# Optimization experiments

Measured on AMD Instinct MI355X. Metric: run time of the kernel, lower is better.

The kernel has to match this reference:

```python
import jax, jax.numpy as jnp
import numpy as np

TOP_K = 4


def setup_inputs() -> dict:
    key = jax.random.key(0)
    k1, k2, k3 = jax.random.split(key, 3)
    T, H, E = 16384, 2880, 128
    hidden_states = jax.random.normal(k1, (T, H), dtype=jnp.float32)
    weight = jax.random.normal(k2, (E, H), dtype=jnp.float32) * 0.02
    bias = jax.random.normal(k3, (E,), dtype=jnp.float32) * 0.02
    return {"hidden_states": hidden_states, "weight": weight, "bias": bias}


def reference(hidden_states, weight, bias):
    # [T, H] @ [H, E] + [E] -> router logits [T, E]
    hidden_states = hidden_states.reshape(-1, weight.shape[1])
    router_logits = jnp.einsum('th,eh->te', hidden_states, weight) + bias
    # top-k over experts, then softmax over the k selected logits
    router_top_value, router_indices = jax.lax.top_k(router_logits, TOP_K)
    router_scores = jax.nn.softmax(router_top_value, axis=-1)
    return router_scores, router_indices
```

## Files before the change

### kernel.cpp

```cpp
#include <hip/hip_runtime.h>
#include <hip/hip_bf16.h>
#include <math.h>

#define T_TOKENS 16384
#define H_DIM    2880
#define KHALF    1440
#define E_EXP    128
#define TOPK     4
#define MT       32
#define KC       32
#define NCHUNK   (H_DIM / KC)
#define NCHUNK_H (KHALF / KC)
#define EPS_GAP  5e-4f

#define WS_WOFF   64
#define WS_WBYTES (NCHUNK * 1024 * 16)
#define WS_FLOFF  (WS_WOFF + WS_WBYTES)
#define WS_NEED   (WS_FLOFF + T_TOKENS * 4)

typedef __bf16 bf16x8 __attribute__((ext_vector_type(8)));
typedef float  f32x4  __attribute__((ext_vector_type(4)));

__device__ __forceinline__ void split2(float a, float b,
                                       unsigned int& hi, unsigned int& lo) {
    float2 p; p.x = a; p.y = b;
    __hip_bfloat162 h = __float22bfloat162_rn(p);
    unsigned int hu; __builtin_memcpy(&hu, &h, 4);
    float2 r;
    r.x = a - __uint_as_float((hu & 0xffffu) << 16);
    r.y = b - __uint_as_float(hu & 0xffff0000u);
    __hip_bfloat162 l = __float22bfloat162_rn(r);
    unsigned int lu; __builtin_memcpy(&lu, &l, 4);
    hi = hu; lo = lu;
}

__global__ __launch_bounds__(256) void prep_w(const float* __restrict__ W,
                                              uint4* __restrict__ wsW) {
    const int f   = blockIdx.x * 256 + threadIdx.x;
    const int kc  = f >> 9;
    const int rem = f & 511;
    const int nt  = rem >> 6;
    const int L   = rem & 63;
    const int e   = nt * 16 + (L & 15);
    const int k   = kc * KC + (L >> 4) * 8;
    const float* p = W + (size_t)e * H_DIM + k;
    const float4 x0 = *(const float4*)p;
    const float4 x1 = *(const float4*)(p + 4);
    uint4 hi, lo;
    split2(x0.x, x0.y, hi.x, lo.x);
    split2(x0.z, x0.w, hi.y, lo.y);
    split2(x1.x, x1.y, hi.z, lo.z);
    split2(x1.z, x1.w, hi.w, lo.w);
    wsW[(size_t)kc * 1024 + nt * 64 + L]       = hi;
    wsW[(size_t)kc * 1024 + 512 + nt * 64 + L] = lo;
}

__global__ __launch_bounds__(512, 4) void router_main(
    const float* __restrict__ A, const uint4* __restrict__ wsW,
    const float* __restrict__ bias, float* __restrict__ out,
    int* __restrict__ flag_count, int* __restrict__ flag_list)
{
    union SMem {
        struct {
            uint4 W  [2][2][1024];
            uint4 Ahi[2][2][2][64];
            uint4 Alo[2][2][2][64];
        } s;
        float L[MT][129];
    };
    __shared__ SMem sm;

    const int tid    = threadIdx.x;
    const int t_base = blockIdx.x * MT;

    const int wave  = tid >> 6;
    const int L     = tid & 63;
    const int whalf = wave >> 2;
    const int wm    = wave & 1;
    const int wn    = (wave >> 1) & 1;

    const int shalf = tid >> 8;
    const int wv    = wave & 3;
    const uint4* wsrc = wsW + (size_t)(shalf * NCHUNK_H) * 1024 + (wv * 4) * 64 + L;

    const bool doA = tid < 256;
    const int at   = tid & 31;
    const int ac   = (tid >> 5) & 7;
    const int ah   = ac >> 2;
    const int akq  = ac & 3;
    const int awm  = at >> 4;
    const int aL   = (akq << 4) | (at & 15);
    const float* Ag = A + (size_t)(t_base + at) * H_DIM + ah * KHALF + akq * 8;

    f32x4 acc[4];
#pragma unroll
    for (int i = 0; i < 4; ++i) { f32x4 z = {0.f, 0.f, 0.f, 0.f}; acc[i] = z; }

#define STAGE(NB, IT)                                                          \
    {                                                                          \
        if (doA) {                                                             \
            uint4 hi4, lo4;                                                    \
            split2(av0.x, av0.y, hi4.x, lo4.x);                                \
            split2(av0.z, av0.w, hi4.y, lo4.y);                                \
            split2(av1.x, av1.y, hi4.z, lo4.z);                                \
            split2(av1.z, av1.w, hi4.w, lo4.w);                                \
            sm.s.Ahi[NB][ah][awm][aL] = hi4;                                   \
            sm.s.Alo[NB][ah][awm][aL] = lo4;                                   \
        }                                                                      \
        const uint4* wc = wsrc + (size_t)(IT) * 1024;                          \
        _Pragma("unroll")                                                      \
        for (int j = 0; j < 4; ++j) {                                          \
            __builtin_amdgcn_global_load_lds(                                  \
                (const __attribute__((address_space(1))) void*)(wc + j * 64),  \
                (__attribute__((address_space(3))) void*)&sm.s.W[NB][shalf][(wv * 4 + j) * 64], \
                16, 0, 0);                                                     \
        }                                                                      \
    }

    float4 av0, av1;
    if (doA) { av0 = *(const float4*)(Ag); av1 = *(const float4*)(Ag + 4); }
    STAGE(0, 0);
    if (doA) { av0 = *(const float4*)(Ag + KC); av1 = *(const float4*)(Ag + KC + 4); }
    __syncthreads();

    int b = 0;
    for (int it = 0; it < NCHUNK_H; ++it) {
        if (it + 1 < NCHUNK_H) {
            STAGE(b ^ 1, it + 1);
            if (doA && it + 2 < NCHUNK_H) {
                av0 = *(const float4*)(Ag + (it + 2) * KC);
                av1 = *(const float4*)(Ag + (it + 2) * KC + 4);
            }
        }
        const bf16x8 ahi = *(const bf16x8*)&sm.s.Ahi[b][whalf][wm][L];
        const bf16x8 alo = *(const bf16x8*)&sm.s.Alo[b][whalf][wm][L];
#pragma unroll
        for (int i = 0; i < 4; ++i) {
            const int nt = wn * 4 + i;
            const bf16x8 whi = *(const bf16x8*)&sm.s.W[b][whalf][nt * 64 + L];
            const bf16x8 wlo = *(const bf16x8*)&sm.s.W[b][whalf][512 + nt * 64 + L];
            acc[i] = __builtin_amdgcn_mfma_f32_16x16x32_bf16(ahi, whi, acc[i], 0, 0, 0);
            acc[i] = __builtin_amdgcn_mfma_f32_16x16x32_bf16(ahi, wlo, acc[i], 0, 0, 0);
            acc[i] = __builtin_amdgcn_mfma_f32_16x16x32_bf16(alo, whi, acc[i], 0, 0, 0);
        }
        __syncthreads();
        b ^= 1;
    }
#undef STAGE

    if (whalf == 0) {
#pragma unroll
        for (int i = 0; i < 4; ++i) {
            const int e = wn * 64 + i * 16 + (L & 15);
            const float bv = bias[e];
#pragma unroll
            for (int r = 0; r < 4; ++r)
                sm.L[wm * 16 + (L >> 4) * 4 + r][e] = acc[i][r] + bv;
        }
    }
    __syncthreads();
    if (whalf == 1) {
#pragma unroll
        for (int i = 0; i < 4; ++i) {
            const int e = wn * 64 + i * 16 + (L & 15);
#pragma unroll
            for (int r = 0; r < 4; ++r)
                sm.L[wm * 16 + (L >> 4) * 4 + r][e] += acc[i][r];
        }
    }
    __syncthreads();

    if (tid < MT) {
        float v0 = -1e30f, v1 = -1e30f, v2 = -1e30f, v3 = -1e30f, v4 = -1e30f;
        int   i0 = 0, i1 = 0, i2 = 0, i3 = 0, i4 = 0;
        for (int e = 0; e < E_EXP; ++e) {
            const float x = sm.L[tid][e];
            if (x > v4) {
                if (x > v0)      { v4=v3;i4=i3; v3=v2;i3=i2; v2=v1;i2=i1; v1=v0;i1=i0; v0=x;i0=e; }
                else if (x > v1) { v4=v3;i4=i3; v3=v2;i3=i2; v2=v1;i2=i1; v1=x;i1=e; }
                else if (x > v2) { v4=v3;i4=i3; v3=v2;i3=i2; v2=x;i2=e; }
                else if (x > v3) { v4=v3;i4=i3; v3=x;i3=e; }
                else             { v4=x;i4=e; }
            }
        }
        const float g0 = v0 - v1, g1 = v1 - v2, g2 = v2 - v3, g3 = v3 - v4;
        float mg = g0 < g1 ? g0 : g1;
        mg = mg < g2 ? mg : g2;
        mg = mg < g3 ? mg : g3;

        const float e0x = expf(v0 - v0);
        const float e1x = expf(v1 - v0);
        const float e2x = expf(v2 - v0);
        const float e3x = expf(v3 - v0);
        const float s   = e0x + e1x + e2x + e3x;

        const int gt = t_base + tid;
        float* out_scores = out;
        float* out_idx    = out + (size_t)T_TOKENS * TOPK;
        out_scores[gt * 4 + 0] = e0x / s;
        out_scores[gt * 4 + 1] = e1x / s;
        out_scores[gt * 4 + 2] = e2x / s;
        out_scores[gt * 4 + 3] = e3x / s;
        out_idx[gt * 4 + 0] = (float)i0;
        out_idx[gt * 4 + 1] = (float)i1;
        out_idx[gt * 4 + 2] = (float)i2;
        out_idx[gt * 4 + 3] = (float)i3;

        if (mg < EPS_GAP) {
            const int p = atomicAdd(flag_count, 1);
            if (p < T_TOKENS) flag_list[p] = gt;
        }
    }
}

__global__ __launch_bounds__(512, 4) void router_main_fb(
    const float* __restrict__ A, const float* __restrict__ W,
    const float* __restrict__ bias, float* __restrict__ out,
    int* __restrict__ flag_count, int* __restrict__ flag_list)
{
    __shared__ __align__(16) uint2 sAhi[2][2][128];
    __shared__ __align__(16) uint2 sAlo[2][2][128];
    __shared__ __align__(16) uint4 sWhi[2][8][64];
    __shared__ __align__(16) uint4 sWlo[2][8][64];
    __shared__ float sL[MT][129];

    const int tid    = threadIdx.x;
    const int t_base = blockIdx.x * MT;
    const int wave  = tid >> 6;
    const int L     = tid & 63;
    const int whalf = wave >> 2;
    const int wm    = wave & 1;
    const int wn    = (wave >> 1) & 1;
    const int shalf = tid >> 8;
    const int tid_h = tid & 255;
    const int at = tid_h >> 3;
    const int ac = tid_h & 7;
    const int a_idx = (at >> 4) * 128 + ((((ac >> 1) << 4) | (at & 15)) << 1) + (ac & 1);
    const float* Ag = A + (size_t)(t_base + at) * H_DIM + shalf * KHALF + ac * 4;
    const int we  = tid_h >> 1;
    const int wq0 = (tid_h & 1) * 2;
    const float* Wg = W + (size_t)we * H_DIM + shalf * KHALF + wq0 * 8;
    const int w_nt = we >> 4;
    const int w_n  = we & 15;

    uint2* sAhiF = &sAhi[shalf][0][0];
    uint2* sAloF = &sAlo[shalf][0][0];

    f32x4 acc[4];
#pragma unroll
    for (int i = 0; i < 4; ++i) { f32x4 z = {0.f, 0.f, 0.f, 0.f}; acc[i] = z; }

    for (int k0 = 0; k0 < KHALF; k0 += KC) {
        const float4 av  = *(const float4*)(Ag + k0);
        const float4 wv0 = *(const float4*)(Wg + k0);
        const float4 wv1 = *(const float4*)(Wg + k0 + 4);
        const float4 wv2 = *(const float4*)(Wg + k0 + 8);
        const float4 wv3 = *(const float4*)(Wg + k0 + 12);

        uint2 ahp, alp;
        split2(av.x, av.y, ahp.x, alp.x);
        split2(av.z, av.w, ahp.y, alp.y);
        uint4 whp0, wlp0, whp1, wlp1;
        split2(wv0.x, wv0.y, whp0.x, wlp0.x);
        split2(wv0.z, wv0.w, whp0.y, wlp0.y);
        split2(wv1.x, wv1.y, whp0.z, wlp0.z);
        split2(wv1.z, wv1.w, whp0.w, wlp0.w);
        split2(wv2.x, wv2.y, whp1.x, wlp1.x);
        split2(wv2.z, wv2.w, whp1.y, wlp1.y);
        split2(wv3.x, wv3.y, whp1.z, wlp1.z);
        split2(wv3.z, wv3.w, whp1.w, wlp1.w);

        __syncthreads();
        sAhiF[a_idx] = ahp;
        sAloF[a_idx] = alp;
        sWhi[shalf][w_nt][((wq0 + 0) << 4) | w_n] = whp0;
        sWhi[shalf][w_nt][((wq0 + 1) << 4) | w_n] = whp1;
        sWlo[shalf][w_nt][((wq0 + 0) << 4) | w_n] = wlp0;
        sWlo[shalf][w_nt][((wq0 + 1) << 4) | w_n] = wlp1;
        __syncthreads();

        const bf16x8 ahi = *(const bf16x8*)&sAhi[whalf][wm][L * 2];
        const bf16x8 alo = *(const bf16x8*)&sAlo[whalf][wm][L * 2];
#pragma unroll
        for (int i = 0; i < 4; ++i) {
            const int nt = wn * 4 + i;
            const bf16x8 whi = *(const bf16x8*)&sWhi[whalf][nt][L];
            const bf16x8 wlo = *(const bf16x8*)&sWlo[whalf][nt][L];
            acc[i] = __builtin_amdgcn_mfma_f32_16x16x32_bf16(ahi, whi, acc[i], 0, 0, 0);
            acc[i] = __builtin_amdgcn_mfma_f32_16x16x32_bf16(ahi, wlo, acc[i], 0, 0, 0);
            acc[i] = __builtin_amdgcn_mfma_f32_16x16x32_bf16(alo, whi, acc[i], 0, 0, 0);
        }
    }

    __syncthreads();
    if (whalf == 0) {
#pragma unroll
        for (int i = 0; i < 4; ++i) {
            const int e = wn * 64 + i * 16 + (L & 15);
            const float b = bias[e];
#pragma unroll
            for (int r = 0; r < 4; ++r)
                sL[wm * 16 + (L >> 4) * 4 + r][e] = acc[i][r] + b;
        }
    }
    __syncthreads();
    if (whalf == 1) {
#pragma unroll
        for (int i = 0; i < 4; ++i) {
            const int e = wn * 64 + i * 16 + (L & 15);
#pragma unroll
            for (int r = 0; r < 4; ++r)
                sL[wm * 16 + (L >> 4) * 4 + r][e] += acc[i][r];
        }
    }
    __syncthreads();

    if (tid < MT) {
        float v0 = -1e30f, v1 = -1e30f, v2 = -1e30f, v3 = -1e30f, v4 = -1e30f;
        int   i0 = 0, i1 = 0, i2 = 0, i3 = 0, i4 = 0;
        for (int e = 0; e < E_EXP; ++e) {
            const float x = sL[tid][e];
            if (x > v4) {
                if (x > v0)      { v4=v3;i4=i3; v3=v2;i3=i2; v2=v1;i2=i1; v1=v0;i1=i0; v0=x;i0=e; }
                else if (x > v1) { v4=v3;i4=i3; v3=v2;i3=i2; v2=v1;i2=i1; v1=x;i1=e; }
                else if (x > v2) { v4=v3;i4=i3; v3=v2;i3=i2; v2=x;i2=e; }
                else if (x > v3) { v4=v3;i4=i3; v3=x;i3=e; }
                else             { v4=x;i4=e; }
            }
        }
        const float g0 = v0 - v1, g1 = v1 - v2, g2 = v2 - v3, g3 = v3 - v4;
        float mg = g0 < g1 ? g0 : g1;
        mg = mg < g2 ? mg : g2;
        mg = mg < g3 ? mg : g3;

        const float e0x = expf(v0 - v0);
        const float e1x = expf(v1 - v0);
        const float e2x = expf(v2 - v0);
        const float e3x = expf(v3 - v0);
        const float s   = e0x + e1x + e2x + e3x;

        const int gt = t_base + tid;
        float* out_scores = out;
        float* out_idx    = out + (size_t)T_TOKENS * TOPK;
        out_scores[gt * 4 + 0] = e0x / s;
        out_scores[gt * 4 + 1] = e1x / s;
        out_scores[gt * 4 + 2] = e2x / s;
        out_scores[gt * 4 + 3] = e3x / s;
        out_idx[gt * 4 + 0] = (float)i0;
        out_idx[gt * 4 + 1] = (float)i1;
        out_idx[gt * 4 + 2] = (float)i2;
        out_idx[gt * 4 + 3] = (float)i3;

        if (mg < EPS_GAP) {
            const int p = atomicAdd(flag_count, 1);
            if (p < T_TOKENS) flag_list[p] = gt;
        }
    }
}

__global__ __launch_bounds__(256) void router_recheck(
    const float* __restrict__ A, const float* __restrict__ W,
    const float* __restrict__ bias, float* __restrict__ out,
    const int* __restrict__ flag_count, const int* __restrict__ flag_list)
{
    __shared__ double sPart[256];
    __shared__ double sLog[E_EXP];

    int count = *flag_count;
    if (count > T_TOKENS) count = T_TOKENS;

    const int tid = threadIdx.x;
    const int e   = tid & (E_EXP - 1);
    const int h   = tid >> 7;

    for (int i = blockIdx.x; i < count; i += gridDim.x) {
        const int t = flag_list[i];
        const float* arow = A + (size_t)t * H_DIM + h * KHALF;
        const float* wrow = W + (size_t)e * H_DIM + h * KHALF;

        double s0 = 0.0, s1 = 0.0, s2 = 0.0, s3 = 0.0;
        float4 a[8], w[8];
#pragma unroll
        for (int q = 0; q < 8; ++q) {
            a[q] = *(const float4*)(arow + q * 4);
            w[q] = *(const float4*)(wrow + q * 4);
        }
        for (int it = 0; it < KHALF / 32 - 1; ++it) {
            const float* ap = arow + (it + 1) * 32;
            const float* wp = wrow + (it + 1) * 32;
            float4 na[8], nw[8];
#pragma unroll
            for (int q = 0; q < 8; ++q) {
                na[q] = *(const float4*)(ap + q * 4);
                nw[q] = *(const float4*)(wp + q * 4);
            }
#pragma unroll
            for (int q = 0; q < 8; ++q) {
                s0 += (double)a[q].x * (double)w[q].x;
                s1 += (double)a[q].y * (double)w[q].y;
                s2 += (double)a[q].z * (double)w[q].z;
                s3 += (double)a[q].w * (double)w[q].w;
            }
#pragma unroll
            for (int q = 0; q < 8; ++q) { a[q] = na[q]; w[q] = nw[q]; }
        }
#pragma unroll
        for (int q = 0; q < 8; ++q) {
            s0 += (double)a[q].x * (double)w[q].x;
            s1 += (double)a[q].y * (double)w[q].y;
            s2 += (double)a[q].z * (double)w[q].z;
            s3 += (double)a[q].w * (double)w[q].w;
        }
        sPart[tid] = (s0 + s1) + (s2 + s3);
        __syncthreads();
        if (h == 0) sLog[e] = sPart[e] + sPart[e + 128] + (double)bias[e];
        __syncthreads();

        if (tid == 0) {
            double v0 = -1e300, v1 = -1e300, v2 = -1e300, v3 = -1e300;
            int    i0 = 0, i1 = 0, i2 = 0, i3 = 0;
            for (int q = 0; q < E_EXP; ++q) {
                const double x = sLog[q];
                if (x > v3) {
                    if (x > v0)      { v3=v2;i3=i2; v2=v1;i2=i1; v1=v0;i1=i0; v0=x;i0=q; }
                    else if (x > v1) { v3=v2;i3=i2; v2=v1;i2=i1; v1=x;i1=q; }
                    else if (x > v2) { v3=v2;i3=i2; v2=x;i2=q; }
                    else             { v3=x;i3=q; }
                }
            }
            const double e0x = exp(v0 - v0);
            const double e1x = exp(v1 - v0);
            const double e2x = exp(v2 - v0);
            const double e3x = exp(v3 - v0);
            const double s   = e0x + e1x + e2x + e3x;
            float* out_scores = out;
            float* out_idx    = out + (size_t)T_TOKENS * TOPK;
            out_scores[t * 4 + 0] = (float)(e0x / s);
            out_scores[t * 4 + 1] = (float)(e1x / s);
            out_scores[t * 4 + 2] = (float)(e2x / s);
            out_scores[t * 4 + 3] = (float)(e3x / s);
            out_idx[t * 4 + 0] = (float)i0;
            out_idx[t * 4 + 1] = (float)i1;
            out_idx[t * 4 + 2] = (float)i2;
            out_idx[t * 4 + 3] = (float)i3;
        }
        __syncthreads();
    }
}

extern "C" void kernel_launch(void* const* d_in, const int* in_sizes, int n_in,
                              void* d_out, int out_size, void* d_ws, size_t ws_size,
                              hipStream_t stream) {
    const float* A    = (const float*)d_in[0];
    const float* W    = (const float*)d_in[1];
    const float* bias = (const float*)d_in[2];
    float* out = (float*)d_out;

    if (ws_size >= (size_t)WS_NEED) {
        int*  flag_count = (int*)d_ws;
        int*  flag_list  = (int*)((char*)d_ws + WS_FLOFF);
        uint4* wsW       = (uint4*)((char*)d_ws + WS_WOFF);
        hipMemsetAsync(flag_count, 0, sizeof(int), stream);
        prep_w<<<dim3((NCHUNK * 512) / 256), dim3(256), 0, stream>>>(W, wsW);
        router_main<<<dim3(T_TOKENS / MT), dim3(512), 0, stream>>>(A, wsW, bias, out,
                                                                   flag_count, flag_list);
        router_recheck<<<dim3(512), dim3(256), 0, stream>>>(A, W, bias, out,
                                                            flag_count, flag_list);
    } else {
        int* flag_count = (int*)d_ws;
        int* flag_list  = (int*)d_ws + 1;
        hipMemsetAsync(flag_count, 0, sizeof(int), stream);
        router_main_fb<<<dim3(T_TOKENS / MT), dim3(512), 0, stream>>>(A, W, bias, out,
                                                                      flag_count, flag_list);
        router_recheck<<<dim3(512), dim3(256), 0, stream>>>(A, W, bias, out,
                                                            flag_count, flag_list);
    }
}
```

Measured before the change: 379.7 us.

## Double router tile to 64 tokens with 1024-thread blocks and 2x2 MFMA warp tiles

```diff
diff --git a/kernel.cpp b/kernel.cpp
--- a/kernel.cpp
+++ b/kernel.cpp
@@ -8,6 +8,7 @@
 #define E_EXP    128
 #define TOPK     4
 #define MT       32
+#define MTM      64
 #define KC       32
 #define NCHUNK   (H_DIM / KC)
 #define NCHUNK_H (KHALF / KC)
@@ -55,7 +56,7 @@
     wsW[(size_t)kc * 1024 + 512 + nt * 64 + L] = lo;
 }
 
-__global__ __launch_bounds__(512, 4) void router_main(
+__global__ __launch_bounds__(1024, 4) void router_main(
     const float* __restrict__ A, const uint4* __restrict__ wsW,
     const float* __restrict__ bias, float* __restrict__ out,
     int* __restrict__ flag_count, int* __restrict__ flag_list)
@@ -63,38 +64,40 @@
     union SMem {
         struct {
             uint4 W  [2][2][1024];
-            uint4 Ahi[2][2][2][64];
-            uint4 Alo[2][2][2][64];
+            uint4 Ahi[2][2][4][64];
+            uint4 Alo[2][2][4][64];
         } s;
-        float L[MT][129];
+        float L[MTM][129];
     };
     __shared__ SMem sm;
 
     const int tid    = threadIdx.x;
-    const int t_base = blockIdx.x * MT;
+    const int t_base = blockIdx.x * MTM;
 
     const int wave  = tid >> 6;
     const int L     = tid & 63;
-    const int whalf = wave >> 2;
-    const int wm    = wave & 1;
-    const int wn    = (wave >> 1) & 1;
-
-    const int shalf = tid >> 8;
-    const int wv    = wave & 3;
-    const uint4* wsrc = wsW + (size_t)(shalf * NCHUNK_H) * 1024 + (wv * 4) * 64 + L;
-
-    const bool doA = tid < 256;
-    const int at   = tid & 31;
-    const int ac   = (tid >> 5) & 7;
+    const int whalf = wave >> 3;
+    const int wmg   = (wave >> 2) & 1;
+    const int wng   = wave & 3;
+
+    const int shalf = whalf;
+    const int wv    = wave & 7;
+    const uint4* wsrc = wsW + (size_t)(shalf * NCHUNK_H) * 1024 + (wv * 2) * 64 + L;
+
+    const bool doA = tid < 512;
+    const int at   = (tid >> 3) & 63;
+    const int ac   = tid & 7;
     const int ah   = ac >> 2;
     const int akq  = ac & 3;
     const int awm  = at >> 4;
     const int aL   = (akq << 4) | (at & 15);
     const float* Ag = A + (size_t)(t_base + at) * H_DIM + ah * KHALF + akq * 8;
 
-    f32x4 acc[4];
-#pragma unroll
-    for (int i = 0; i < 4; ++i) { f32x4 z = {0.f, 0.f, 0.f, 0.f}; acc[i] = z; }
+    f32x4 acc[2][2];
+#pragma unroll
+    for (int m = 0; m < 2; ++m)
+#pragma unroll
+        for (int n = 0; n < 2; ++n) { f32x4 z = {0.f, 0.f, 0.f, 0.f}; acc[m][n] = z; }
 
 #define STAGE(NB, IT)                                                          \
     {                                                                          \
@@ -109,10 +112,10 @@
         }                                                                      \
         const uint4* wc = wsrc + (size_t)(IT) * 1024;                          \
         _Pragma("unroll")                                                      \
-        for (int j = 0; j < 4; ++j) {                                          \
+        for (int j = 0; j < 2; ++j) {                                          \
             __builtin_amdgcn_global_load_lds(                                  \
                 (const __attribute__((address_space(1))) void*)(wc + j * 64),  \
-                (__attribute__((address_space(3))) void*)&sm.s.W[NB][shalf][(wv * 4 + j) * 64], \
+                (__attribute__((address_space(3))) void*)&sm.s.W[NB][shalf][(wv * 2 + j) * 64], \
                 16, 0, 0);                                                     \
         }                                                                      \
     }
@@ -132,16 +135,21 @@
                 av1 = *(const float4*)(Ag + (it + 2) * KC + 4);
             }
         }
-        const bf16x8 ahi = *(const bf16x8*)&sm.s.Ahi[b][whalf][wm][L];
-        const bf16x8 alo = *(const bf16x8*)&sm.s.Alo[b][whalf][wm][L];
-#pragma unroll
-        for (int i = 0; i < 4; ++i) {
-            const int nt = wn * 4 + i;
+        const bf16x8 ah0 = *(const bf16x8*)&sm.s.Ahi[b][whalf][wmg * 2 + 0][L];
+        const bf16x8 al0 = *(const bf16x8*)&sm.s.Alo[b][whalf][wmg * 2 + 0][L];
+        const bf16x8 ah1 = *(const bf16x8*)&sm.s.Ahi[b][whalf][wmg * 2 + 1][L];
+        const bf16x8 al1 = *(const bf16x8*)&sm.s.Alo[b][whalf][wmg * 2 + 1][L];
+#pragma unroll
+        for (int n = 0; n < 2; ++n) {
+            const int nt = wng * 2 + n;
             const bf16x8 whi = *(const bf16x8*)&sm.s.W[b][whalf][nt * 64 + L];
             const bf16x8 wlo = *(const bf16x8*)&sm.s.W[b][whalf][512 + nt * 64 + L];
-            acc[i] = __builtin_amdgcn_mfma_f32_16x16x32_bf16(ahi, whi, acc[i], 0, 0, 0);
-            acc[i] = __builtin_amdgcn_mfma_f32_16x16x32_bf16(ahi, wlo, acc[i], 0, 0, 0);
-            acc[i] = __builtin_amdgcn_mfma_f32_16x16x32_bf16(alo, whi, acc[i], 0, 0, 0);
+            acc[0][n] = __builtin_amdgcn_mfma_f32_16x16x32_bf16(ah0, whi, acc[0][n], 0, 0, 0);
+            acc[0][n] = __builtin_amdgcn_mfma_f32_16x16x32_bf16(ah0, wlo, acc[0][n], 0, 0, 0);
+            acc[0][n] = __builtin_amdgcn_mfma_f32_16x16x32_bf16(al0, whi, acc[0][n], 0, 0, 0);
+            acc[1][n] = __builtin_amdgcn_mfma_f32_16x16x32_bf16(ah1, whi, acc[1][n], 0, 0, 0);
+            acc[1][n] = __builtin_amdgcn_mfma_f32_16x16x32_bf16(ah1, wlo, acc[1][n], 0, 0, 0);
+            acc[1][n] = __builtin_amdgcn_mfma_f32_16x16x32_bf16(al1, whi, acc[1][n], 0, 0, 0);
         }
         __syncthreads();
         b ^= 1;
@@ -150,27 +158,31 @@
 
     if (whalf == 0) {
 #pragma unroll
-        for (int i = 0; i < 4; ++i) {
-            const int e = wn * 64 + i * 16 + (L & 15);
-            const float bv = bias[e];
-#pragma unroll
-            for (int r = 0; r < 4; ++r)
-                sm.L[wm * 16 + (L >> 4) * 4 + r][e] = acc[i][r] + bv;
-        }
+        for (int m = 0; m < 2; ++m)
+#pragma unroll
+            for (int n = 0; n < 2; ++n) {
+                const int e = (wng * 2 + n) * 16 + (L & 15);
+                const float bv = bias[e];
+#pragma unroll
+                for (int r = 0; r < 4; ++r)
+                    sm.L[(wmg * 2 + m) * 16 + (L >> 4) * 4 + r][e] = acc[m][n][r] + bv;
+            }
     }
     __syncthreads();
     if (whalf == 1) {
 #pragma unroll
-        for (int i = 0; i < 4; ++i) {
-            const int e = wn * 64 + i * 16 + (L & 15);
-#pragma unroll
-            for (int r = 0; r < 4; ++r)
-                sm.L[wm * 16 + (L >> 4) * 4 + r][e] += acc[i][r];
-        }
-    }
-    __syncthreads();
-
-    if (tid < MT) {
+        for (int m = 0; m < 2; ++m)
+#pragma unroll
+            for (int n = 0; n < 2; ++n) {
+                const int e = (wng * 2 + n) * 16 + (L & 15);
+#pragma unroll
+                for (int r = 0; r < 4; ++r)
+                    sm.L[(wmg * 2 + m) * 16 + (L >> 4) * 4 + r][e] += acc[m][n][r];
+            }
+    }
+    __syncthreads();
+
+    if (tid < MTM) {
         float v0 = -1e30f, v1 = -1e30f, v2 = -1e30f, v3 = -1e30f, v4 = -1e30f;
         int   i0 = 0, i1 = 0, i2 = 0, i3 = 0, i4 = 0;
         for (int e = 0; e < E_EXP; ++e) {
@@ -462,8 +474,8 @@
         uint4* wsW       = (uint4*)((char*)d_ws + WS_WOFF);
         hipMemsetAsync(flag_count, 0, sizeof(int), stream);
         prep_w<<<dim3((NCHUNK * 512) / 256), dim3(256), 0, stream>>>(W, wsW);
-        router_main<<<dim3(T_TOKENS / MT), dim3(512), 0, stream>>>(A, wsW, bias, out,
-                                                                   flag_count, flag_list);
+        router_main<<<dim3(T_TOKENS / MTM), dim3(1024), 0, stream>>>(A, wsW, bias, out,
+                                                                     flag_count, flag_list);
         router_recheck<<<dim3(512), dim3(256), 0, stream>>>(A, W, bias, out,
                                                             flag_count, flag_list);
     } else {
```

Result: no change. 374.5 us (-1.4%).
